# Optimization experiments

Measured on AMD Instinct MI355X. Metric: run time of the kernel, lower is better.

Reference implementation:

```python
import jax, jax.numpy as jnp
import numpy as np

E, T, D, H = 8, 2048, 1024, 4096  # experts, tokens/expert, n_embed, n_mlp_hidden


def setup_inputs() -> dict:
    key = jax.random.key(0)
    ks = jax.random.split(key, 4)
    return {
        "x": jax.random.normal(ks[0], (E, T, D), dtype=jnp.float32),
        "w_c_fc": jax.random.normal(ks[1], (E, D, H), dtype=jnp.float32) * 0.02,
        "b_c_fc": jnp.zeros((E, 1, H), dtype=jnp.float32),
        "w_gate": jax.random.normal(ks[2], (E, D, H), dtype=jnp.float32) * 0.02,
        "b_gate": jnp.zeros((E, 1, H), dtype=jnp.float32),
        "w_c_proj": jax.random.normal(ks[3], (E, H, D), dtype=jnp.float32) * (0.02 * (2 * 12) ** -0.5),
        "b_c_proj": jnp.zeros((E, 1, D), dtype=jnp.float32),
    }


def reference(x, w_c_fc, b_c_fc, w_gate, b_gate, w_c_proj, b_c_proj):
    # Per-expert batched GEMMs with gated activation: silu(h * g)
    h = jnp.einsum('eti,eih->eth', x, w_c_fc) + b_c_fc
    g = jnp.einsum('eti,eih->eth', x, w_gate) + b_gate
    o = jnp.einsum('eth,eho->eto', jax.nn.silu(h * g), w_c_proj) + b_c_proj
    return o
```

## Files before the change

### kernel.cpp

```cpp
#include <hip/hip_runtime.h>
#include <hip/hip_bf16.h>
#include <stdint.h>


#define T_ 2048
#define D_ 1024
#define H_ 4096
#define NE 8

typedef unsigned short u16;
typedef __attribute__((ext_vector_type(8))) u16 u16x8;
typedef __attribute__((ext_vector_type(4))) u16 u16x4;
typedef __attribute__((ext_vector_type(8))) short bf16x8;
typedef __attribute__((ext_vector_type(4))) float f32x4;

__device__ __forceinline__ uint32_t bf16_rne(float f) {
    union { float f; uint32_t u; } v; v.f = f;
    return (v.u + 0x7FFFu + ((v.u >> 16) & 1u)) >> 16;
}

__device__ __forceinline__ void gload16(const void* g, void* l) {
    __builtin_amdgcn_global_load_lds((const __attribute__((address_space(1))) void*)g,
                                     (__attribute__((address_space(3))) void*)l,
                                     16, 0, 0);
}

#define SBAR() __builtin_amdgcn_s_barrier()

__global__ __launch_bounds__(256) void tobf16_kernel(const float* __restrict__ in,
    u16* __restrict__ oh, int n4) {
    int i = blockIdx.x * 256 + threadIdx.x;
    if (i >= n4) return;
    float4 v = reinterpret_cast<const float4*>(in)[i];
    float c[4] = {v.x, v.y, v.z, v.w};
    u16x4 h{};
#pragma unroll
    for (int j = 0; j < 4; ++j) h[j] = (u16)bf16_rne(c[j]);
    reinterpret_cast<u16x4*>(oh)[i] = h;
}

__global__ __launch_bounds__(256) void transpose_hi_kernel(
    const float* __restrict__ in, u16* __restrict__ oh, int R, int C) {
    __shared__ float tile[64][65];
    const int z = blockIdx.z;
    const int r0 = blockIdx.x * 64, c0 = blockIdx.y * 64;
    const float* src = in + (size_t)z * R * C;
    const int tr = threadIdx.x >> 4;
    const int tc = (threadIdx.x & 15) * 4;
#pragma unroll
    for (int j = 0; j < 4; ++j) {
        const float4 v = *reinterpret_cast<const float4*>(&src[(size_t)(r0 + tr + j*16) * C + c0 + tc]);
        tile[tr + j*16][tc+0] = v.x; tile[tr + j*16][tc+1] = v.y;
        tile[tr + j*16][tc+2] = v.z; tile[tr + j*16][tc+3] = v.w;
    }
    __syncthreads();
    const int cl = threadIdx.x & 63;
    const int q  = threadIdx.x >> 6;
    u16x8 h0{}, h1{};
#pragma unroll
    for (int rr = 0; rr < 8; ++rr) h0[rr] = (u16)bf16_rne(tile[q*16 + rr][cl]);
#pragma unroll
    for (int rr = 0; rr < 8; ++rr) h1[rr] = (u16)bf16_rne(tile[q*16 + 8 + rr][cl]);
    size_t ob = ((size_t)z * C + c0 + cl) * R + r0 + q*16;
    *reinterpret_cast<u16x8*>(&oh[ob])     = h0;
    *reinterpret_cast<u16x8*>(&oh[ob + 8]) = h1;
}


template<bool PF, int VM>
__device__ __forceinline__ void fc_step(int tt, u16 (&sm)[4][16384],
    const u16* asrc, const u16* bsrc, const u16* gsrc,
    int adst0, int adst1, int bdst, int gdst,
    int aoff, int boff, int goff,
    f32x4 (&acch)[4][4], f32x4 (&accg)[4][4])
{
    const u16* sb = &sm[tt & 3][0];
    u16* db = &sm[(tt + 3) & 3][0];
    bf16x8 Af[4], Bf[4], Gf[4];
#pragma unroll
    for (int i = 0; i < 4; ++i) Af[i] = *(const bf16x8*)(sb + aoff + i * 512);
#pragma unroll
    for (int i = 0; i < 4; ++i) Bf[i] = *(const bf16x8*)(sb + boff + i * 512);
    if (PF) {
        gload16(asrc + (tt + 3) * 32, db + adst0);
        gload16(asrc + (tt + 3) * 32 + (size_t)16 * D_, db + adst1);
    }
    SBAR();
    __builtin_amdgcn_s_setprio(1);
#pragma unroll
    for (int mi = 0; mi < 4; ++mi)
#pragma unroll
        for (int ni = 0; ni < 4; ++ni)
            acch[mi][ni] = __builtin_amdgcn_mfma_f32_16x16x32_bf16(Af[mi], Bf[ni], acch[mi][ni], 0, 0, 0);
    __builtin_amdgcn_s_setprio(0);
    SBAR();
#pragma unroll
    for (int i = 0; i < 4; ++i) Gf[i] = *(const bf16x8*)(sb + goff + i * 512);
    if (PF) {
        gload16(bsrc + (tt + 3) * 32, db + bdst);
        gload16(gsrc + (tt + 3) * 32, db + gdst);
    }
    if (VM == 8)      asm volatile("s_waitcnt vmcnt(8)" ::: "memory");
    else if (VM == 4) asm volatile("s_waitcnt vmcnt(4)" ::: "memory");
    else if (VM == 0) asm volatile("s_waitcnt vmcnt(0)" ::: "memory");
    SBAR();
    __builtin_amdgcn_s_setprio(1);
#pragma unroll
    for (int mi = 0; mi < 4; ++mi)
#pragma unroll
        for (int ni = 0; ni < 4; ++ni)
            accg[mi][ni] = __builtin_amdgcn_mfma_f32_16x16x32_bf16(Af[mi], Gf[ni], accg[mi][ni], 0, 0, 0);
    __builtin_amdgcn_s_setprio(0);
    SBAR();
}

__global__ __launch_bounds__(512, 2) void gemm_fc_gate(
    const u16* __restrict__ xh, const u16* __restrict__ fh, const u16* __restrict__ gh,
    const float* __restrict__ bfc, const float* __restrict__ bgt,
    u16* __restrict__ act)
{
    __shared__ __align__(16) u16 sm[4][16384];
    const int z  = blockIdx.z;
    const int m0 = blockIdx.x * 256;
    const int n0 = blockIdx.y * 128;
    const int tid = threadIdx.x;
    const int lane = tid & 63;
    const int wid = tid >> 6;
    const int wr = wid >> 1;
    const int wc = wid & 1;

    const u16* asrc = xh + ((size_t)z * T_ + m0 + wid * 32 + (lane >> 2)) * D_ + (lane & 3) * 8;
    const u16* bsrc = fh + ((size_t)z * H_ + n0 + wid * 16 + (lane >> 2)) * D_ + (lane & 3) * 8;
    const u16* gsrc = gh + ((size_t)z * H_ + n0 + wid * 16 + (lane >> 2)) * D_ + (lane & 3) * 8;
    const int adst0 = wid * 1024;
    const int adst1 = adst0 + 512;
    const int bdst  = 8192 + wid * 512;
    const int gdst  = 12288 + wid * 512;

    const int aoff = (wr * 64 + (lane & 15)) * 32 + (lane >> 4) * 8;
    const int boff = 8192 + (wc * 64 + (lane & 15)) * 32 + (lane >> 4) * 8;
    const int goff = boff + 4096;

    f32x4 acch[4][4], accg[4][4];
#pragma unroll
    for (int i = 0; i < 4; ++i)
#pragma unroll
        for (int j = 0; j < 4; ++j) {
            acch[i][j] = (f32x4){0.f, 0.f, 0.f, 0.f};
            accg[i][j] = (f32x4){0.f, 0.f, 0.f, 0.f};
        }

#pragma unroll
    for (int u = 0; u < 3; ++u) {
        u16* db = &sm[u][0];
        gload16(asrc + u * 32, db + adst0);
        gload16(asrc + u * 32 + (size_t)16 * D_, db + adst1);
        gload16(bsrc + u * 32, db + bdst);
        gload16(gsrc + u * 32, db + gdst);
    }
    asm volatile("s_waitcnt vmcnt(8)" ::: "memory");
    SBAR();

#pragma unroll 4
    for (int t = 0; t < 29; ++t)
        fc_step<true, 8>(t, sm, asrc, bsrc, gsrc, adst0, adst1, bdst, gdst, aoff, boff, goff, acch, accg);
    fc_step<false, 4>(29, sm, asrc, bsrc, gsrc, adst0, adst1, bdst, gdst, aoff, boff, goff, acch, accg);
    fc_step<false, 0>(30, sm, asrc, bsrc, gsrc, adst0, adst1, bdst, gdst, aoff, boff, goff, acch, accg);
    fc_step<false, -1>(31, sm, asrc, bsrc, gsrc, adst0, adst1, bdst, gdst, aoff, boff, goff, acch, accg);

#pragma unroll
    for (int mi = 0; mi < 4; ++mi) {
#pragma unroll
        for (int ni = 0; ni < 4; ++ni) {
            const int col = n0 + wc * 64 + ni * 16 + (lane & 15);
            const float bh = bfc[(size_t)z * H_ + col];
            const float bg = bgt[(size_t)z * H_ + col];
#pragma unroll
            for (int r = 0; r < 4; ++r) {
                const int row = m0 + wr * 64 + mi * 16 + (lane >> 4) * 4 + r;
                float h = acch[mi][ni][r] + bh;
                float g = accg[mi][ni][r] + bg;
                float zz = h * g;
                float s = zz / (1.0f + __expf(-zz));
                act[((size_t)z * T_ + row) * H_ + col] = (u16)bf16_rne(s);
            }
        }
    }
}


template<bool PF, int VM>
__device__ __forceinline__ void pj_step(int tt, u16 (&sm)[4][12288],
    const u16* asrc, const u16* bsrc,
    int adst0, int adst1, int bdst, int aoff, int boff,
    f32x4 (&acc)[4][4])
{
    const u16* sb = &sm[tt & 3][0];
    u16* db = &sm[(tt + 3) & 3][0];
    bf16x8 Af[4], Bf[4];
#pragma unroll
    for (int i = 0; i < 4; ++i) Af[i] = *(const bf16x8*)(sb + aoff + i * 512);
#pragma unroll
    for (int i = 0; i < 4; ++i) Bf[i] = *(const bf16x8*)(sb + boff + i * 512);
    if (PF) {
        gload16(asrc + (tt + 3) * 32, db + adst0);
        gload16(asrc + (tt + 3) * 32 + (size_t)16 * H_, db + adst1);
        gload16(bsrc + (tt + 3) * 32, db + bdst);
    }
    if (VM == 6)      asm volatile("s_waitcnt vmcnt(6)" ::: "memory");
    else if (VM == 3) asm volatile("s_waitcnt vmcnt(3)" ::: "memory");
    else if (VM == 0) asm volatile("s_waitcnt vmcnt(0)" ::: "memory");
    SBAR();
    __builtin_amdgcn_s_setprio(1);
#pragma unroll
    for (int mi = 0; mi < 4; ++mi)
#pragma unroll
        for (int ni = 0; ni < 4; ++ni)
            acc[mi][ni] = __builtin_amdgcn_mfma_f32_16x16x32_bf16(Af[mi], Bf[ni], acc[mi][ni], 0, 0, 0);
    __builtin_amdgcn_s_setprio(0);
    SBAR();
}

__global__ __launch_bounds__(512, 2) void gemm_proj(
    const u16* __restrict__ act, const u16* __restrict__ ph,
    const float* __restrict__ bp, float* __restrict__ out)
{
    __shared__ __align__(16) u16 sm[4][12288];
    const int z  = blockIdx.z;
    const int m0 = blockIdx.x * 256;
    const int n0 = blockIdx.y * 128;
    const int tid = threadIdx.x;
    const int lane = tid & 63;
    const int wid = tid >> 6;
    const int wr = wid >> 1;
    const int wc = wid & 1;

    const u16* asrc = act + ((size_t)z * T_ + m0 + wid * 32 + (lane >> 2)) * H_ + (lane & 3) * 8;
    const u16* bsrc = ph  + ((size_t)z * D_ + n0 + wid * 16 + (lane >> 2)) * H_ + (lane & 3) * 8;
    const int adst0 = wid * 1024;
    const int adst1 = adst0 + 512;
    const int bdst  = 8192 + wid * 512;

    const int aoff = (wr * 64 + (lane & 15)) * 32 + (lane >> 4) * 8;
    const int boff = 8192 + (wc * 64 + (lane & 15)) * 32 + (lane >> 4) * 8;

    f32x4 acc[4][4];
#pragma unroll
    for (int i = 0; i < 4; ++i)
#pragma unroll
        for (int j = 0; j < 4; ++j) acc[i][j] = (f32x4){0.f, 0.f, 0.f, 0.f};

#pragma unroll
    for (int u = 0; u < 3; ++u) {
        u16* db = &sm[u][0];
        gload16(asrc + u * 32, db + adst0);
        gload16(asrc + u * 32 + (size_t)16 * H_, db + adst1);
        gload16(bsrc + u * 32, db + bdst);
    }
    asm volatile("s_waitcnt vmcnt(6)" ::: "memory");
    SBAR();

#pragma unroll 4
    for (int t = 0; t < 125; ++t)
        pj_step<true, 6>(t, sm, asrc, bsrc, adst0, adst1, bdst, aoff, boff, acc);
    pj_step<false, 3>(125, sm, asrc, bsrc, adst0, adst1, bdst, aoff, boff, acc);
    pj_step<false, 0>(126, sm, asrc, bsrc, adst0, adst1, bdst, aoff, boff, acc);
    pj_step<false, -1>(127, sm, asrc, bsrc, adst0, adst1, bdst, aoff, boff, acc);

#pragma unroll
    for (int mi = 0; mi < 4; ++mi) {
#pragma unroll
        for (int ni = 0; ni < 4; ++ni) {
            const int col = n0 + wc * 64 + ni * 16 + (lane & 15);
            const float bv = bp[(size_t)z * D_ + col];
#pragma unroll
            for (int r = 0; r < 4; ++r) {
                const int row = m0 + wr * 64 + mi * 16 + (lane >> 4) * 4 + r;
                out[((size_t)z * T_ + row) * D_ + col] = acc[mi][ni][r] + bv;
            }
        }
    }
}

extern "C" void kernel_launch(void* const* d_in, const int* in_sizes, int n_in,
                              void* d_out, int out_size, void* d_ws, size_t ws_size,
                              hipStream_t stream) {
    const float* x   = (const float*)d_in[0];
    const float* wfc = (const float*)d_in[1];
    const float* bfc = (const float*)d_in[2];
    const float* wg  = (const float*)d_in[3];
    const float* bg  = (const float*)d_in[4];
    const float* wp  = (const float*)d_in[5];
    const float* bp  = (const float*)d_in[6];
    float* out = (float*)d_out;

    const size_t per_e = ((size_t)T_*D_ + 3*(size_t)D_*H_ + (size_t)T_*H_) * 2;
    int EB = (int)(ws_size / per_e);
    if (EB < 1) EB = 1;
    if (EB > NE) EB = NE;

    for (int e0 = 0; e0 < NE; e0 += EB) {
        const int eb = (NE - e0 < EB) ? (NE - e0) : EB;
        char* p = (char*)d_ws;
        u16* xh = (u16*)p; p += (size_t)eb*T_*D_*2;
        u16* fh = (u16*)p; p += (size_t)eb*D_*H_*2;
        u16* gh = (u16*)p; p += (size_t)eb*D_*H_*2;
        u16* ph = (u16*)p; p += (size_t)eb*H_*D_*2;
        u16* act = (u16*)p;

        const int n4 = eb * T_ * D_ / 4;
        tobf16_kernel<<<dim3((n4 + 255) / 256), 256, 0, stream>>>(
            x + (size_t)e0*T_*D_, xh, n4);
        transpose_hi_kernel<<<dim3(D_/64, H_/64, eb), 256, 0, stream>>>(
            wfc + (size_t)e0*D_*H_, fh, D_, H_);
        transpose_hi_kernel<<<dim3(D_/64, H_/64, eb), 256, 0, stream>>>(
            wg + (size_t)e0*D_*H_, gh, D_, H_);
        transpose_hi_kernel<<<dim3(H_/64, D_/64, eb), 256, 0, stream>>>(
            wp + (size_t)e0*H_*D_, ph, H_, D_);
        gemm_fc_gate<<<dim3(T_/256, H_/128, eb), 512, 0, stream>>>(
            xh, fh, gh, bfc + (size_t)e0*H_, bg + (size_t)e0*H_, act);
        gemm_proj<<<dim3(T_/256, D_/128, eb), 512, 0, stream>>>(
            act, ph, bp + (size_t)e0*D_, out + (size_t)e0*T_*D_);
    }
}
```

Measured before the change: 640.2 us.

## Swizzle LDS layout, remap block order, and cut barriers in MoE GEMMs

Applies an XOR swizzle to the column chunk used by both the global-to-LDS loads and the fragment reads, so the ds_reads spread across LDS banks instead of conflicting. Remaps block indices so that consecutively launched blocks share weight tiles, aiming for better L2 reuse. Merges barriers by moving one to the start of each k-step and issuing the gate fragment reads before the first MFMA batch, which reduces the number of synchronisations per step. Replaces the SiLU division with a hardware reciprocal. The main risks are correctness of the reduced barrier ordering in the 4-stage ring buffer and whether the grid-mapping assumptions hold.

```diff
diff --git a/kernel.cpp b/kernel.cpp
--- a/kernel.cpp
+++ b/kernel.cpp
@@ -74,6 +74,7 @@
     int aoff, int boff, int goff,
     f32x4 (&acch)[4][4], f32x4 (&accg)[4][4])
 {
+    SBAR();
     const u16* sb = &sm[tt & 3][0];
     u16* db = &sm[(tt + 3) & 3][0];
     bf16x8 Af[4], Bf[4], Gf[4];
@@ -85,7 +86,8 @@
         gload16(asrc + (tt + 3) * 32, db + adst0);
         gload16(asrc + (tt + 3) * 32 + (size_t)16 * D_, db + adst1);
     }
-    SBAR();
+#pragma unroll
+    for (int i = 0; i < 4; ++i) Gf[i] = *(const bf16x8*)(sb + goff + i * 512);
     __builtin_amdgcn_s_setprio(1);
 #pragma unroll
     for (int mi = 0; mi < 4; ++mi)
@@ -93,9 +95,6 @@
         for (int ni = 0; ni < 4; ++ni)
             acch[mi][ni] = __builtin_amdgcn_mfma_f32_16x16x32_bf16(Af[mi], Bf[ni], acch[mi][ni], 0, 0, 0);
     __builtin_amdgcn_s_setprio(0);
-    SBAR();
-#pragma unroll
-    for (int i = 0; i < 4; ++i) Gf[i] = *(const bf16x8*)(sb + goff + i * 512);
     if (PF) {
         gload16(bsrc + (tt + 3) * 32, db + bdst);
         gload16(gsrc + (tt + 3) * 32, db + gdst);
@@ -111,7 +110,6 @@
         for (int ni = 0; ni < 4; ++ni)
             accg[mi][ni] = __builtin_amdgcn_mfma_f32_16x16x32_bf16(Af[mi], Gf[ni], accg[mi][ni], 0, 0, 0);
     __builtin_amdgcn_s_setprio(0);
-    SBAR();
 }
 
 __global__ __launch_bounds__(512, 2) void gemm_fc_gate(
@@ -121,24 +119,28 @@
 {
     __shared__ __align__(16) u16 sm[4][16384];
     const int z  = blockIdx.z;
-    const int m0 = blockIdx.x * 256;
-    const int n0 = blockIdx.y * 128;
+    const int lin = blockIdx.x + (blockIdx.y << 3);
+    const int swz = ((lin & 7) << 5) + (lin >> 3);
+    const int m0 = (swz & 7) * 256;
+    const int n0 = (swz >> 3) * 128;
     const int tid = threadIdx.x;
     const int lane = tid & 63;
     const int wid = tid >> 6;
     const int wr = wid >> 1;
     const int wc = wid & 1;
 
-    const u16* asrc = xh + ((size_t)z * T_ + m0 + wid * 32 + (lane >> 2)) * D_ + (lane & 3) * 8;
-    const u16* bsrc = fh + ((size_t)z * H_ + n0 + wid * 16 + (lane >> 2)) * D_ + (lane & 3) * 8;
-    const u16* gsrc = gh + ((size_t)z * H_ + n0 + wid * 16 + (lane >> 2)) * D_ + (lane & 3) * 8;
+    const int cs = ((lane & 3) ^ ((lane >> 3) & 3)) * 8;
+    const u16* asrc = xh + ((size_t)z * T_ + m0 + wid * 32 + (lane >> 2)) * D_ + cs;
+    const u16* bsrc = fh + ((size_t)z * H_ + n0 + wid * 16 + (lane >> 2)) * D_ + cs;
+    const u16* gsrc = gh + ((size_t)z * H_ + n0 + wid * 16 + (lane >> 2)) * D_ + cs;
     const int adst0 = wid * 1024;
     const int adst1 = adst0 + 512;
     const int bdst  = 8192 + wid * 512;
     const int gdst  = 12288 + wid * 512;
 
-    const int aoff = (wr * 64 + (lane & 15)) * 32 + (lane >> 4) * 8;
-    const int boff = 8192 + (wc * 64 + (lane & 15)) * 32 + (lane >> 4) * 8;
+    const int cswz = (((lane & 15) >> 1) & 3);
+    const int aoff = (wr * 64 + (lane & 15)) * 32 + ((lane >> 4) ^ cswz) * 8;
+    const int boff = 8192 + (wc * 64 + (lane & 15)) * 32 + ((lane >> 4) ^ cswz) * 8;
     const int goff = boff + 4096;
 
     f32x4 acch[4][4], accg[4][4];
@@ -159,7 +161,6 @@
         gload16(gsrc + u * 32, db + gdst);
     }
     asm volatile("s_waitcnt vmcnt(8)" ::: "memory");
-    SBAR();
 
 #pragma unroll 4
     for (int t = 0; t < 29; ++t)
@@ -181,7 +182,7 @@
                 float h = acch[mi][ni][r] + bh;
                 float g = accg[mi][ni][r] + bg;
                 float zz = h * g;
-                float s = zz / (1.0f + __expf(-zz));
+                float s = zz * __builtin_amdgcn_rcpf(1.0f + __expf(-zz));
                 act[((size_t)z * T_ + row) * H_ + col] = (u16)bf16_rne(s);
             }
         }
@@ -195,6 +196,7 @@
     int adst0, int adst1, int bdst, int aoff, int boff,
     f32x4 (&acc)[4][4])
 {
+    SBAR();
     const u16* sb = &sm[tt & 3][0];
     u16* db = &sm[(tt + 3) & 3][0];
     bf16x8 Af[4], Bf[4];
@@ -218,7 +220,6 @@
         for (int ni = 0; ni < 4; ++ni)
             acc[mi][ni] = __builtin_amdgcn_mfma_f32_16x16x32_bf16(Af[mi], Bf[ni], acc[mi][ni], 0, 0, 0);
     __builtin_amdgcn_s_setprio(0);
-    SBAR();
 }
 
 __global__ __launch_bounds__(512, 2) void gemm_proj(
@@ -227,22 +228,26 @@
 {
     __shared__ __align__(16) u16 sm[4][12288];
     const int z  = blockIdx.z;
-    const int m0 = blockIdx.x * 256;
-    const int n0 = blockIdx.y * 128;
+    const int lin = blockIdx.x + (blockIdx.y << 3);
+    const int swz = ((lin & 7) << 3) + (lin >> 3);
+    const int m0 = (swz & 7) * 256;
+    const int n0 = (swz >> 3) * 128;
     const int tid = threadIdx.x;
     const int lane = tid & 63;
     const int wid = tid >> 6;
     const int wr = wid >> 1;
     const int wc = wid & 1;
 
-    const u16* asrc = act + ((size_t)z * T_ + m0 + wid * 32 + (lane >> 2)) * H_ + (lane & 3) * 8;
-    const u16* bsrc = ph  + ((size_t)z * D_ + n0 + wid * 16 + (lane >> 2)) * H_ + (lane & 3) * 8;
+    const int cs = ((lane & 3) ^ ((lane >> 3) & 3)) * 8;
+    const u16* asrc = act + ((size_t)z * T_ + m0 + wid * 32 + (lane >> 2)) * H_ + cs;
+    const u16* bsrc = ph  + ((size_t)z * D_ + n0 + wid * 16 + (lane >> 2)) * H_ + cs;
     const int adst0 = wid * 1024;
     const int adst1 = adst0 + 512;
     const int bdst  = 8192 + wid * 512;
 
-    const int aoff = (wr * 64 + (lane & 15)) * 32 + (lane >> 4) * 8;
-    const int boff = 8192 + (wc * 64 + (lane & 15)) * 32 + (lane >> 4) * 8;
+    const int cswz = (((lane & 15) >> 1) & 3);
+    const int aoff = (wr * 64 + (lane & 15)) * 32 + ((lane >> 4) ^ cswz) * 8;
+    const int boff = 8192 + (wc * 64 + (lane & 15)) * 32 + ((lane >> 4) ^ cswz) * 8;
 
     f32x4 acc[4][4];
 #pragma unroll
@@ -258,7 +263,6 @@
         gload16(bsrc + u * 32, db + bdst);
     }
     asm volatile("s_waitcnt vmcnt(6)" ::: "memory");
-    SBAR();
 
 #pragma unroll 4
     for (int t = 0; t < 125; ++t)
```

New measurement: 616.0 us. -3.8%, faster.
